# Optimization experiments

Hardware: AMD Instinct MI355X
Metric: run time of the kernel (lower is better)

Reference implementation:

```python
import jax, jax.numpy as jnp
import numpy as np

BATCH, IN_DIM, LATENT, K = 16384, 768, 12288, 32

def setup_inputs() -> dict:
    key = jax.random.key(0)
    k1, k2, k3 = jax.random.split(key, 3)
    # kaiming-uniform-style scale for encoder/decoder weights
    enc_bound = float(np.sqrt(6.0 / IN_DIM))
    dec_bound = float(np.sqrt(6.0 / LATENT))
    x = jax.random.normal(k1, (BATCH, IN_DIM), dtype=jnp.float32)
    enc_w = jax.random.uniform(k2, (LATENT, IN_DIM), dtype=jnp.float32, minval=-enc_bound, maxval=enc_bound)
    enc_b = jnp.zeros((LATENT,), dtype=jnp.float32)
    dec_w = jax.random.uniform(k3, (IN_DIM, LATENT), dtype=jnp.float32, minval=-dec_bound, maxval=dec_bound)
    dec_b = jnp.zeros((IN_DIM,), dtype=jnp.float32)
    return {"x": x, "enc_w": enc_w, "enc_b": enc_b, "dec_w": dec_w, "dec_b": dec_b, "k": K}

def reference(x, enc_w, enc_b, dec_w, dec_b, k):
    # encode: z = x @ W_e^T + b_e            [B, LATENT]
    z = jnp.einsum('bi,li->bl', x, enc_w) + enc_b
    # top-k threshold: kth largest value per row, then shifted relu
    vals, _ = jax.lax.top_k(z, k)
    thresh = vals[:, -1:]                     # [B, 1]
    z_sparse = jax.nn.relu(z - thresh)
    # decode: dense GEMM over all latent columns (as in original module)
    x_recon = jnp.einsum('bl,il->bi', z_sparse, dec_w) + dec_b
    return (x_recon, z_sparse)
```

## Files before the change

kernel.cpp:

```cpp
#include <hip/hip_runtime.h>

#define M_DIM 16384
#define K_DIM 768
#define N_DIM 12288
#define TOPK  32

typedef float f32x4 __attribute__((ext_vector_type(4)));
typedef short s16x8 __attribute__((ext_vector_type(8)));

__device__ __forceinline__ unsigned f2u(float f) {
  union { float f; unsigned u; } v; v.f = f; return v.u;
}
__device__ __forceinline__ float u2f(unsigned u) {
  union { unsigned u; float f; } v; v.u = u; return v.f;
}

__device__ __forceinline__ unsigned short bf16_rne(float f) {
  unsigned u = f2u(f);
  return (unsigned short)((u + 0x7FFFu + ((u >> 16) & 1u)) >> 16);
}

__global__ __launch_bounds__(256) void split_bf16_planes(
    const float* __restrict__ src, unsigned short* __restrict__ hi,
    unsigned short* __restrict__ lo, int n4)
{
  const int stride = (int)(gridDim.x * blockDim.x);
  for (int i = (int)(blockIdx.x * blockDim.x + threadIdx.x); i < n4; i += stride) {
    const float4 v = ((const float4*)src)[i];
    ushort4 h, l;
    h.x = bf16_rne(v.x); h.y = bf16_rne(v.y); h.z = bf16_rne(v.z); h.w = bf16_rne(v.w);
    l.x = bf16_rne(v.x - u2f((unsigned)h.x << 16));
    l.y = bf16_rne(v.y - u2f((unsigned)h.y << 16));
    l.z = bf16_rne(v.z - u2f((unsigned)h.z << 16));
    l.w = bf16_rne(v.w - u2f((unsigned)h.w << 16));
    ((ushort4*)hi)[i] = h;
    ((ushort4*)lo)[i] = l;
  }
}

__device__ __forceinline__ void mfma16(f32x4& d, s16x8 a, s16x8 b) {
  asm("v_mfma_f32_16x16x32_bf16 %0, %1, %2, %0" : "+v"(d) : "v"(a), "v"(b));
}

#define GL16(g, l) __builtin_amdgcn_global_load_lds(                      \
    (const __attribute__((address_space(1))) void*)(g),                   \
    (__attribute__((address_space(3))) void*)(l), 16, 0, 0)

__global__ __launch_bounds__(256, 2) void TopKSparseAutoencoder_51917564674099_kernel(
    const unsigned short* __restrict__ Ahi, const unsigned short* __restrict__ Alo,
    const unsigned short* __restrict__ Bhi, const unsigned short* __restrict__ Blo,
    const float* __restrict__ bias, float* __restrict__ Z)
{
  __shared__ unsigned short lds[4][128][32];

  const int t    = (int)threadIdx.x;
  const int wid  = t >> 6;
  const int lane = t & 63;

  const int bid  = (int)(blockIdx.y * gridDim.x + blockIdx.x);
  const int bswz = (bid & 7) * (12288 / 8) + (bid >> 3);
  const int n0   = (bswz % 96) * 128;
  const int m0   = (bswz / 96) * 128;

  const int rr  = lane >> 2;
  const int kq  = lane & 3;
  const int rt0 = wid * 32 + rr;
  const int rt1 = rt0 + 16;
  const int kc0 = (kq ^ ((rt0 >> 1) & 3)) * 8;
  const int kc1 = (kq ^ ((rt1 >> 1) & 3)) * 8;
  const size_t offA0 = (size_t)(m0 + rt0) * K_DIM + kc0;
  const size_t offA1 = (size_t)(m0 + rt1) * K_DIM + kc1;
  const size_t offB0 = (size_t)(n0 + rt0) * K_DIM + kc0;
  const size_t offB1 = (size_t)(n0 + rt1) * K_DIM + kc1;

  const int wm = (wid >> 1) * 64;
  const int wn = (wid & 1) * 64;
  const int lr = lane & 15;
  const int lc = lane >> 4;

  f32x4 acc[4][4];
#pragma unroll
  for (int i = 0; i < 4; ++i)
#pragma unroll
    for (int j = 0; j < 4; ++j) acc[i][j] = (f32x4){0.f, 0.f, 0.f, 0.f};

  for (int k0 = 0; k0 < K_DIM; k0 += 32) {
    GL16(Ahi + offA0 + k0, &lds[0][wid * 32][0]);
    GL16(Ahi + offA1 + k0, &lds[0][wid * 32 + 16][0]);
    GL16(Alo + offA0 + k0, &lds[1][wid * 32][0]);
    GL16(Alo + offA1 + k0, &lds[1][wid * 32 + 16][0]);
    GL16(Bhi + offB0 + k0, &lds[2][wid * 32][0]);
    GL16(Bhi + offB1 + k0, &lds[2][wid * 32 + 16][0]);
    GL16(Blo + offB0 + k0, &lds[3][wid * 32][0]);
    GL16(Blo + offB1 + k0, &lds[3][wid * 32 + 16][0]);
    __syncthreads();

    s16x8 ah[4], al[4], bh[4], bl[4];
#pragma unroll
    for (int i = 0; i < 4; ++i) {
      const int r = wm + i * 16 + lr;
      const int p = (lc ^ ((r >> 1) & 3)) * 8;
      ah[i] = *(const s16x8*)&lds[0][r][p];
      al[i] = *(const s16x8*)&lds[1][r][p];
    }
#pragma unroll
    for (int j = 0; j < 4; ++j) {
      const int r = wn + j * 16 + lr;
      const int p = (lc ^ ((r >> 1) & 3)) * 8;
      bh[j] = *(const s16x8*)&lds[2][r][p];
      bl[j] = *(const s16x8*)&lds[3][r][p];
    }
#pragma unroll
    for (int i = 0; i < 4; ++i)
#pragma unroll
      for (int j = 0; j < 4; ++j) {
        mfma16(acc[i][j], ah[i], bh[j]);
        mfma16(acc[i][j], ah[i], bl[j]);
        mfma16(acc[i][j], al[i], bh[j]);
      }
    __syncthreads();
  }

  asm volatile("s_nop 7\n\ts_nop 7" :::);

#pragma unroll
  for (int j = 0; j < 4; ++j) {
    const int col = n0 + wn + j * 16 + lr;
    const float bb = bias[col];
#pragma unroll
    for (int i = 0; i < 4; ++i) {
      const int r0 = m0 + wm + i * 16 + lc * 4;
#pragma unroll
      for (int q = 0; q < 4; ++q)
        Z[(size_t)(r0 + q) * N_DIM + col] = acc[i][j][q] + bb;
    }
  }
}

__global__ void enc_gemm_f32_fb(
    const float* A, const float* B, const float* bias, float* Z)
{
  __shared__ float As[32][132];
  __shared__ float Bs[32][132];

  const int tx = (int)threadIdx.x;
  const int ty = (int)threadIdx.y;
  const int t  = ty * 16 + tx;
  const int n0 = (int)blockIdx.x * 128;
  const int m0 = (int)blockIdx.y * 128;
  const int r = t >> 1;
  const int h = (t & 1) * 16;

  float c[8][8];
#pragma unroll
  for (int i = 0; i < 8; ++i)
#pragma unroll
    for (int j = 0; j < 8; ++j) c[i][j] = 0.0f;

  for (int k0 = 0; k0 < K_DIM; k0 += 32) {
    const float* pa = A + (size_t)(m0 + r) * K_DIM + k0 + h;
    const float* pb = B + (size_t)(n0 + r) * K_DIM + k0 + h;
    float fa[16], fb[16];
#pragma unroll
    for (int j = 0; j < 16; ++j) fa[j] = pa[j];
#pragma unroll
    for (int j = 0; j < 16; ++j) fb[j] = pb[j];
#pragma unroll
    for (int j = 0; j < 16; ++j) As[h + j][r] = fa[j];
#pragma unroll
    for (int j = 0; j < 16; ++j) Bs[h + j][r] = fb[j];
    __syncthreads();

    for (int kk = 0; kk < 32; ++kk) {
      float av[8], bv[8];
#pragma unroll
      for (int i = 0; i < 8; ++i) av[i] = As[kk][ty * 8 + i];
#pragma unroll
      for (int j = 0; j < 8; ++j) bv[j] = Bs[kk][tx * 8 + j];
#pragma unroll
      for (int i = 0; i < 8; ++i)
#pragma unroll
        for (int j = 0; j < 8; ++j) c[i][j] += av[i] * bv[j];
    }
    __syncthreads();
  }

#pragma unroll
  for (int j = 0; j < 8; ++j) {
    const int col = n0 + tx * 8 + j;
    const float bb = bias[col];
#pragma unroll
    for (int i = 0; i < 8; ++i)
      Z[(size_t)(m0 + ty * 8 + i) * N_DIM + col] = c[i][j] + bb;
  }
}

__global__ void transpose_decw(const float* W, float* WT)
{
  __shared__ float tile[32][33];
  const int bx = (int)blockIdx.x;
  const int by = (int)blockIdx.y;
  const int tx = (int)threadIdx.x;
  const int ty = (int)threadIdx.y;
#pragma unroll
  for (int j = 0; j < 32; j += 8)
    tile[ty + j][tx] = W[(size_t)(by * 32 + ty + j) * N_DIM + bx * 32 + tx];
  __syncthreads();
#pragma unroll
  for (int j = 0; j < 32; j += 8)
    WT[(size_t)(bx * 32 + ty + j) * K_DIM + by * 32 + tx] = tile[tx][ty + j];
}

__global__ __launch_bounds__(256, 4) void topk_select_decode(
    float* Z,
    const float* __restrict__ WT,
    const float* __restrict__ DW,
    const float* __restrict__ db,
    float* __restrict__ XR,
    int use_wt)
{
  __shared__ unsigned wcnt[2][4];
  __shared__ int s_nnz;
  __shared__ int   s_col[TOPK];
  __shared__ float s_val[TOPK];

  const int row  = (int)blockIdx.x;
  const int t    = (int)threadIdx.x;
  const int lane = t & 63;
  const int wid  = t >> 6;

  float4* zv = (float4*)(Z + (size_t)row * N_DIM);

  unsigned kk[48];
#pragma unroll
  for (int j = 0; j < 12; ++j) {
    const float4 v = zv[t + 256 * j];
    unsigned u;
    u = f2u(v.x); kk[4 * j + 0] = u ^ (unsigned)(((int)u >> 31) | 0x80000000);
    u = f2u(v.y); kk[4 * j + 1] = u ^ (unsigned)(((int)u >> 31) | 0x80000000);
    u = f2u(v.z); kk[4 * j + 2] = u ^ (unsigned)(((int)u >> 31) | 0x80000000);
    u = f2u(v.w); kk[4 * j + 3] = u ^ (unsigned)(((int)u >> 31) | 0x80000000);
  }
  if (t == 0) s_nnz = 0;

  unsigned lo = 0u, hi = 0xFFFFFFFFu;
  for (int it = 0; it < 32; ++it) {
    const unsigned mid = lo + ((hi - lo) >> 1);
    unsigned c = 0;
#pragma unroll
    for (int q = 0; q < 48; ++q) c += (kk[q] > mid) ? 1u : 0u;
    c += __shfl_down(c, 32);
    c += __shfl_down(c, 16);
    c += __shfl_down(c, 8);
    c += __shfl_down(c, 4);
    c += __shfl_down(c, 2);
    c += __shfl_down(c, 1);
    if (lane == 0) wcnt[it & 1][wid] = c;
    __syncthreads();
    const unsigned tot = wcnt[it & 1][0] + wcnt[it & 1][1] +
                         wcnt[it & 1][2] + wcnt[it & 1][3];
    if (tot >= (unsigned)TOPK) lo = mid; else hi = mid;
  }
  const unsigned T = hi;
  const float thresh = u2f((T & 0x80000000u) ? (T ^ 0x80000000u) : ~T);

#define COMP(Q, FLD) {                                                        \
      const unsigned key = kk[4 * j + Q];                                     \
      float v = 0.0f;                                                         \
      if (key > T) {                                                          \
        v = u2f((key & 0x80000000u) ? (key ^ 0x80000000u) : ~key) - thresh;   \
        const int p = atomicAdd(&s_nnz, 1);                                   \
        if (p < TOPK) { s_col[p] = base + Q; s_val[p] = v; }                  \
      }                                                                       \
      o.FLD = v; }
#pragma unroll
  for (int j = 0; j < 12; ++j) {
    float4 o;
    const int base = (t + 256 * j) * 4;
    COMP(0, x)
    COMP(1, y)
    COMP(2, z)
    COMP(3, w)
    zv[t + 256 * j] = o;
  }
#undef COMP
  __syncthreads();

  const int nnz = (s_nnz < TOPK) ? s_nnz : TOPK;
  float a0 = 0.0f, a1 = 0.0f, a2 = 0.0f;
  if (use_wt) {
    for (int j = 0; j < nnz; ++j) {
      const float v = s_val[j];
      const float* w = WT + (size_t)s_col[j] * K_DIM;
      a0 += v * w[t];
      a1 += v * w[t + 256];
      a2 += v * w[t + 512];
    }
  } else {
    for (int j = 0; j < nnz; ++j) {
      const float v = s_val[j];
      const int col = s_col[j];
      a0 += v * DW[(size_t)(t)       * N_DIM + col];
      a1 += v * DW[(size_t)(t + 256) * N_DIM + col];
      a2 += v * DW[(size_t)(t + 512) * N_DIM + col];
    }
  }
  float* xr = XR + (size_t)row * K_DIM;
  xr[t]       = a0 + db[t];
  xr[t + 256] = a1 + db[t + 256];
  xr[t + 512] = a2 + db[t + 512];
}

extern "C" void kernel_launch(void* const* d_in, const int* in_sizes, int n_in,
                              void* d_out, int out_size, void* d_ws, size_t ws_size,
                              hipStream_t stream)
{
  (void)in_sizes; (void)n_in; (void)out_size;

  const float* x     = (const float*)d_in[0];
  const float* enc_w = (const float*)d_in[1];
  const float* enc_b = (const float*)d_in[2];
  const float* dec_w = (const float*)d_in[3];
  const float* dec_b = (const float*)d_in[4];

  float* out     = (float*)d_out;
  float* x_recon = out;
  float* z_sp    = out + (size_t)M_DIM * K_DIM;

  const size_t WT_BYTES = (size_t)N_DIM * K_DIM * sizeof(float);
  const size_t XPLANE   = (size_t)M_DIM * K_DIM * sizeof(unsigned short);
  const size_t WPLANE   = (size_t)N_DIM * K_DIM * sizeof(unsigned short);
  const size_t FULL     = WT_BYTES + 2 * XPLANE + 2 * WPLANE;

  char* ws = (char*)d_ws;
  const int use_wt   = (ws_size >= WT_BYTES) ? 1 : 0;
  const int use_mfma = (ws_size >= FULL) ? 1 : 0;

  float*          WT  = (float*)ws;
  unsigned short* xhi = (unsigned short*)(ws + WT_BYTES);
  unsigned short* xlo = (unsigned short*)(ws + WT_BYTES + XPLANE);
  unsigned short* whi = (unsigned short*)(ws + WT_BYTES + 2 * XPLANE);
  unsigned short* wlo = (unsigned short*)(ws + WT_BYTES + 2 * XPLANE + WPLANE);

  if (use_wt) {
    dim3 tb(32, 8);
    dim3 tg(N_DIM / 32, K_DIM / 32);
    transpose_decw<<<tg, tb, 0, stream>>>(dec_w, WT);
  }

  if (use_mfma) {
    split_bf16_planes<<<1024, 256, 0, stream>>>(x, xhi, xlo, M_DIM * K_DIM / 4);
    split_bf16_planes<<<1024, 256, 0, stream>>>(enc_w, whi, wlo, N_DIM * K_DIM / 4);
    dim3 tg(N_DIM / 128, M_DIM / 128);
    TopKSparseAutoencoder_51917564674099_kernel<<<tg, 256, 0, stream>>>(
        xhi, xlo, whi, wlo, enc_b, z_sp);
  } else {
    dim3 tb(16, 16);
    dim3 tg(N_DIM / 128, M_DIM / 128);
    enc_gemm_f32_fb<<<tg, tb, 0, stream>>>(x, enc_w, enc_b, z_sp);
  }

  topk_select_decode<<<M_DIM, 256, 0, stream>>>(z_sp, WT, dec_w, dec_b, x_recon, use_wt);
}
```

Baseline: 2.314 ms.

## Use radix-4 threshold search with LDS-staged keys and candidate compaction

Replaces the 32-round binary search over register-held keys with a 4-way search: each round counts keys above three pivots, so 16 rounds cover the 32-bit key space. Keys are staged in shared memory (48KB per block) rather than 48 registers. After 8 full rounds the surviving candidates are compacted into a small list and one wavefront finishes the last 8 rounds with no block barriers. The decode loop is fixed at 32 entries and unrolled. This cuts block-wide barriers and compare work, but shared-memory use lowers occupancy, so the launch bound drops to 3 blocks per CU.

```diff
diff --git a/kernel.cpp b/kernel.cpp
--- a/kernel.cpp
+++ b/kernel.cpp
@@ -13,6 +13,13 @@
 }
 __device__ __forceinline__ float u2f(unsigned u) {
   union { unsigned u; float f; } v; v.u = u; return v.f;
+}
+__device__ __forceinline__ unsigned fkey(float f) {
+  const unsigned u = f2u(f);
+  return u ^ (unsigned)(((int)u >> 31) | 0x80000000);
+}
+__device__ __forceinline__ float kinv(unsigned k) {
+  return u2f((k & 0x80000000u) ? (k ^ 0x80000000u) : ~k);
 }
 
 __device__ __forceinline__ unsigned short bf16_rne(float f) {
@@ -211,7 +218,39 @@
     WT[(size_t)(bx * 32 + ty + j) * K_DIM + by * 32 + tx] = tile[tx][ty + j];
 }
 
-__global__ __launch_bounds__(256, 4) void topk_select_decode(
+__device__ __forceinline__ void full_round(
+    const uint4* zk, unsigned red[][2][4], int t, int lane, int wid, int r,
+    unsigned& lo, unsigned long long& w)
+{
+  w >>= 2;
+  const unsigned wu = (unsigned)w;
+  const unsigned m1 = lo + wu, m2 = lo + 2u * wu, m3 = lo + 3u * wu;
+  unsigned c1 = 0, c2 = 0, c3 = 0;
+#pragma unroll
+  for (int j = 0; j < 12; ++j) {
+    const uint4 k = zk[t + 256 * j];
+    c1 += (k.x >= m1) + (k.y >= m1) + (k.z >= m1) + (k.w >= m1);
+    c2 += (k.x >= m2) + (k.y >= m2) + (k.z >= m2) + (k.w >= m2);
+    c3 += (k.x >= m3) + (k.y >= m3) + (k.z >= m3) + (k.w >= m3);
+  }
+  unsigned p = c1 | (c2 << 16), q = c3;
+  p += __shfl_down(p, 32); q += __shfl_down(q, 32);
+  p += __shfl_down(p, 16); q += __shfl_down(q, 16);
+  p += __shfl_down(p, 8);  q += __shfl_down(q, 8);
+  p += __shfl_down(p, 4);  q += __shfl_down(q, 4);
+  p += __shfl_down(p, 2);  q += __shfl_down(q, 2);
+  p += __shfl_down(p, 1);  q += __shfl_down(q, 1);
+  const int par = r & 1;
+  if (lane == 0) { red[par][0][wid] = p; red[par][1][wid] = q; }
+  __syncthreads();
+  const unsigned P = red[par][0][0] + red[par][0][1] + red[par][0][2] + red[par][0][3];
+  const unsigned Q = red[par][1][0] + red[par][1][1] + red[par][1][2] + red[par][1][3];
+  if (Q >= (unsigned)TOPK)                lo = m3;
+  else if ((P >> 16) >= (unsigned)TOPK)   lo = m2;
+  else if ((P & 0xFFFFu) >= (unsigned)TOPK) lo = m1;
+}
+
+__global__ __launch_bounds__(256, 3) void topk_select_decode(
     float* Z,
     const float* __restrict__ WT,
     const float* __restrict__ DW,
@@ -219,7 +258,11 @@
     float* __restrict__ XR,
     int use_wt)
 {
-  __shared__ unsigned wcnt[2][4];
+  __shared__ uint4 zkey4[N_DIM / 4];
+  __shared__ unsigned red[2][2][4];
+  __shared__ unsigned cand[256];
+  __shared__ unsigned s_T;
+  __shared__ int s_cc;
   __shared__ int s_nnz;
   __shared__ int   s_col[TOPK];
   __shared__ float s_val[TOPK];
@@ -231,73 +274,104 @@
 
   float4* zv = (float4*)(Z + (size_t)row * N_DIM);
 
-  unsigned kk[48];
 #pragma unroll
   for (int j = 0; j < 12; ++j) {
     const float4 v = zv[t + 256 * j];
-    unsigned u;
-    u = f2u(v.x); kk[4 * j + 0] = u ^ (unsigned)(((int)u >> 31) | 0x80000000);
-    u = f2u(v.y); kk[4 * j + 1] = u ^ (unsigned)(((int)u >> 31) | 0x80000000);
-    u = f2u(v.z); kk[4 * j + 2] = u ^ (unsigned)(((int)u >> 31) | 0x80000000);
-    u = f2u(v.w); kk[4 * j + 3] = u ^ (unsigned)(((int)u >> 31) | 0x80000000);
-  }
-  if (t == 0) s_nnz = 0;
-
-  unsigned lo = 0u, hi = 0xFFFFFFFFu;
-  for (int it = 0; it < 32; ++it) {
-    const unsigned mid = lo + ((hi - lo) >> 1);
-    unsigned c = 0;
-#pragma unroll
-    for (int q = 0; q < 48; ++q) c += (kk[q] > mid) ? 1u : 0u;
-    c += __shfl_down(c, 32);
-    c += __shfl_down(c, 16);
-    c += __shfl_down(c, 8);
-    c += __shfl_down(c, 4);
-    c += __shfl_down(c, 2);
-    c += __shfl_down(c, 1);
-    if (lane == 0) wcnt[it & 1][wid] = c;
-    __syncthreads();
-    const unsigned tot = wcnt[it & 1][0] + wcnt[it & 1][1] +
-                         wcnt[it & 1][2] + wcnt[it & 1][3];
-    if (tot >= (unsigned)TOPK) lo = mid; else hi = mid;
-  }
-  const unsigned T = hi;
-  const float thresh = u2f((T & 0x80000000u) ? (T ^ 0x80000000u) : ~T);
-
-#define COMP(Q, FLD) {                                                        \
-      const unsigned key = kk[4 * j + Q];                                     \
+    uint4 k;
+    k.x = fkey(v.x); k.y = fkey(v.y); k.z = fkey(v.z); k.w = fkey(v.w);
+    zkey4[t + 256 * j] = k;
+  }
+  if (t == 0) { s_nnz = 0; s_cc = 0; }
+  if (t < TOPK) { s_col[t] = 0; s_val[t] = 0.0f; }
+  __syncthreads();
+
+  unsigned lo = 0;
+  unsigned long long w = 1ULL << 32;
+  for (int r = 0; r < 8; ++r)
+    full_round(zkey4, red, t, lane, wid, r, lo, w);
+
+#pragma unroll
+  for (int j = 0; j < 12; ++j) {
+    const uint4 k = zkey4[t + 256 * j];
+    if (k.x >= lo) { int p = atomicAdd(&s_cc, 1); if (p < 256) cand[p] = k.x; }
+    if (k.y >= lo) { int p = atomicAdd(&s_cc, 1); if (p < 256) cand[p] = k.y; }
+    if (k.z >= lo) { int p = atomicAdd(&s_cc, 1); if (p < 256) cand[p] = k.z; }
+    if (k.w >= lo) { int p = atomicAdd(&s_cc, 1); if (p < 256) cand[p] = k.w; }
+  }
+  __syncthreads();
+  const int cc = s_cc;
+
+  if (cc <= 256) {
+    if (wid == 0) {
+      const unsigned k0 = (lane       < cc) ? cand[lane]       : 0u;
+      const unsigned k1 = (lane + 64  < cc) ? cand[lane + 64]  : 0u;
+      const unsigned k2 = (lane + 128 < cc) ? cand[lane + 128] : 0u;
+      const unsigned k3 = (lane + 192 < cc) ? cand[lane + 192] : 0u;
+      for (int r = 8; r < 16; ++r) {
+        w >>= 2;
+        const unsigned wu = (unsigned)w;
+        const unsigned m1 = lo + wu, m2 = lo + 2u * wu, m3 = lo + 3u * wu;
+        unsigned c1 = (k0 >= m1) + (k1 >= m1) + (k2 >= m1) + (k3 >= m1);
+        unsigned c2 = (k0 >= m2) + (k1 >= m2) + (k2 >= m2) + (k3 >= m2);
+        unsigned c3 = (k0 >= m3) + (k1 >= m3) + (k2 >= m3) + (k3 >= m3);
+        unsigned p = c1 | (c2 << 16), q = c3;
+        p += __shfl_down(p, 32); q += __shfl_down(q, 32);
+        p += __shfl_down(p, 16); q += __shfl_down(q, 16);
+        p += __shfl_down(p, 8);  q += __shfl_down(q, 8);
+        p += __shfl_down(p, 4);  q += __shfl_down(q, 4);
+        p += __shfl_down(p, 2);  q += __shfl_down(q, 2);
+        p += __shfl_down(p, 1);  q += __shfl_down(q, 1);
+        p = __shfl(p, 0); q = __shfl(q, 0);
+        if (q >= (unsigned)TOPK)                  lo = m3;
+        else if ((p >> 16) >= (unsigned)TOPK)     lo = m2;
+        else if ((p & 0xFFFFu) >= (unsigned)TOPK) lo = m1;
+      }
+      if (lane == 0) s_T = lo;
+    }
+  } else {
+    for (int r = 8; r < 16; ++r)
+      full_round(zkey4, red, t, lane, wid, r, lo, w);
+    if (t == 0) s_T = lo;
+  }
+  __syncthreads();
+  const unsigned T = s_T;
+  const float thresh = kinv(T);
+
+#define COMP(KF, OFS, OF) {                                                   \
       float v = 0.0f;                                                         \
-      if (key > T) {                                                          \
-        v = u2f((key & 0x80000000u) ? (key ^ 0x80000000u) : ~key) - thresh;   \
+      if (KF > T) {                                                           \
+        v = kinv(KF) - thresh;                                                \
         const int p = atomicAdd(&s_nnz, 1);                                   \
-        if (p < TOPK) { s_col[p] = base + Q; s_val[p] = v; }                  \
+        if (p < TOPK) { s_col[p] = base + OFS; s_val[p] = v; }                \
       }                                                                       \
-      o.FLD = v; }
+      o.OF = v; }
 #pragma unroll
   for (int j = 0; j < 12; ++j) {
+    const uint4 k = zkey4[t + 256 * j];
+    const int base = (t + 256 * j) * 4;
     float4 o;
-    const int base = (t + 256 * j) * 4;
-    COMP(0, x)
-    COMP(1, y)
-    COMP(2, z)
-    COMP(3, w)
+    COMP(k.x, 0, x)
+    COMP(k.y, 1, y)
+    COMP(k.z, 2, z)
+    COMP(k.w, 3, w)
     zv[t + 256 * j] = o;
   }
 #undef COMP
   __syncthreads();
 
-  const int nnz = (s_nnz < TOPK) ? s_nnz : TOPK;
   float a0 = 0.0f, a1 = 0.0f, a2 = 0.0f;
   if (use_wt) {
-    for (int j = 0; j < nnz; ++j) {
+#pragma unroll 8
+    for (int j = 0; j < TOPK; ++j) {
       const float v = s_val[j];
-      const float* w = WT + (size_t)s_col[j] * K_DIM;
-      a0 += v * w[t];
-      a1 += v * w[t + 256];
-      a2 += v * w[t + 512];
+      const float* wp = WT + (size_t)s_col[j] * K_DIM;
+      a0 += v * wp[t];
+      a1 += v * wp[t + 256];
+      a2 += v * wp[t + 512];
     }
   } else {
-    for (int j = 0; j < nnz; ++j) {
+#pragma unroll 8
+    for (int j = 0; j < TOPK; ++j) {
       const float v = s_val[j];
       const int col = s_col[j];
       a0 += v * DW[(size_t)(t)       * N_DIM + col];
```

Measured after the change: 2.410 ms. 4.2% more time.
